# Optimization experiments

Measured on AMD Instinct MI355X. Metric: run time of the kernel, lower is better.

The kernel has to match this reference:

```python
import jax, jax.numpy as jnp
import numpy as np

N, E, D, H = 50000, 800000, 128, 8
C = D // H  # head dim = 16

def _layer_norm(x, g, b, eps=1e-5):
    mu = jnp.mean(x, axis=-1, keepdims=True)
    var = jnp.var(x, axis=-1, keepdims=True)
    return (x - mu) * jax.lax.rsqrt(var + eps) * g + b

def setup_inputs() -> dict:
    key = jax.random.key(0)
    ks = jax.random.split(key, 24)
    def lin(i, fan_in=D):
        s = 1.0 / np.sqrt(fan_in)
        return (jax.random.uniform(ks[i], (D, D), minval=-s, maxval=s),
                jax.random.uniform(ks[i + 1], (D,), minval=-s, maxval=s))
    Wq, bq = lin(0); Wk, bk = lin(2); Wv, bv = lin(4)
    We, be = lin(6); Ws, bs = lin(8)
    W1, b1 = lin(10); W2, b2 = lin(12)
    return {
        'edge_index': jax.random.randint(ks[14], (2, E), 0, N),
        'node_attr': jax.random.normal(ks[15], (N, D), dtype=jnp.float32),
        'edge_attr': jax.random.normal(ks[16], (E, D), dtype=jnp.float32),
        'Wq': Wq, 'bq': bq, 'Wk': Wk, 'bk': bk, 'Wv': Wv, 'bv': bv,
        'We': We, 'be': be, 'Ws': Ws, 'bs': bs,
        'W1': W1, 'b1': b1, 'W2': W2, 'b2': b2,
        'ln1_g': jnp.ones((D,)), 'ln1_b': jnp.zeros((D,)),
        'ln2_g': jnp.ones((D,)), 'ln2_b': jnp.zeros((D,)),
    }

def _transformer_conv(node_attr, edge_attr, src, dst, Wq, bq, Wk, bk, Wv, bv, We, be, Ws, bs):
    # PyG TransformerConv, concat=True, root_weight=True, beta=False, eval (no dropout)
    q = (node_attr @ Wq.T + bq).reshape(N, H, C)[dst]          # [E,H,C]
    e = (edge_attr @ We.T + be).reshape(E, H, C)               # [E,H,C]
    k = (node_attr @ Wk.T + bk).reshape(N, H, C)[src] + e      # [E,H,C]
    v = (node_attr @ Wv.T + bv).reshape(N, H, C)[src] + e      # [E,H,C]
    alpha = jnp.sum(q * k, axis=-1) / jnp.sqrt(jnp.float32(C)) # [E,H]
    # segment softmax over destination node
    m = jax.ops.segment_max(alpha, dst, num_segments=N)        # [N,H]
    ex = jnp.exp(alpha - m[dst])
    denom = jax.ops.segment_sum(ex, dst, num_segments=N)       # [N,H]
    a = ex / (denom[dst] + 1e-16)                              # [E,H]
    out = jax.ops.segment_sum(v * a[..., None], dst, num_segments=N)  # [N,H,C]
    out = out.reshape(N, D)
    return out + node_attr @ Ws.T + bs  # root/skip connection

def reference(edge_index, node_attr, edge_attr, Wq, bq, Wk, bk, Wv, bv, We, be,
              Ws, bs, W1, b1, W2, b2, ln1_g, ln1_b, ln2_g, ln2_b):
    src, dst = edge_index[0], edge_index[1]
    x = _transformer_conv(node_attr, edge_attr, src, dst,
                          Wq, bq, Wk, bk, Wv, bv, We, be, Ws, bs)
    node_attr = node_attr + _layer_norm(x, ln1_g, ln1_b)
    h = jax.nn.silu(node_attr @ W1.T + b1) @ W2.T + b2
    node_attr = node_attr + _layer_norm(h, ln2_g, ln2_b)
    return node_attr
```

## Files before the change

### kernel.cpp

```cpp
#include <hip/hip_runtime.h>
#include <hip/hip_fp16.h>

#define N_NODES 50000
#define N_EDGES 800000
#define DIM 128
#define NODE_TILES 782
#define EDGE_TILES 12500
#define SCAN_NB 50

typedef _Float16 f16;
typedef _Float16 f16x2 __attribute__((ext_vector_type(2)));
typedef _Float16 f16x4 __attribute__((ext_vector_type(4)));
typedef _Float16 f16x8 __attribute__((ext_vector_type(8)));
typedef float    f32x16 __attribute__((ext_vector_type(16)));

__device__ __forceinline__ void sfence() { __builtin_amdgcn_sched_barrier(0); }

__device__ __forceinline__ void load_wfrag(const f16* __restrict__ Wh, int ch, int l31, int g,
                                           f16x8 bf[2][8]) {
#pragma unroll
  for (int c = 0; c < 2; ++c)
#pragma unroll
    for (int ks = 0; ks < 8; ++ks)
      bf[c][ks] = *(const f16x8*)(Wh + ((ch * 64 + c * 32 + l31) << 7) + 16 * ks + 8 * g);
}

__device__ __forceinline__ void stage_issue(const float* __restrict__ X, long M, long base,
                                            int tid, float4 sv[8]) {
#pragma unroll
  for (int kk = 0; kk < 8; ++kk) {
    int i = tid + kk * 256;
    long row = base + (i >> 5);
    long gr = row < M ? row : (M - 1);
    sv[kk] = *(const float4*)(X + gr * DIM + (i & 31) * 4);
  }
}

__device__ __forceinline__ void stage_write(const float4 sv[8], int tid, f16* __restrict__ lds) {
#pragma unroll
  for (int kk = 0; kk < 8; ++kk) {
    int i = tid + kk * 256;
    int r = i >> 5, s8 = i & 31;
    f16x4 h;
    h[0] = (f16)sv[kk].x; h[1] = (f16)sv[kk].y; h[2] = (f16)sv[kk].z; h[3] = (f16)sv[kk].w;
    *(f16x4*)(lds + r * 128 + (((s8 >> 1) ^ (r & 15)) << 3) + ((s8 & 1) << 2)) = h;
  }
}

__device__ __forceinline__ void mfma_lds_g(const f16* __restrict__ A, int lr, int g,
                                           const f16x8 bf[2][8], f32x16 acc[2]) {
#pragma unroll
  for (int c = 0; c < 2; ++c)
#pragma unroll
    for (int k = 0; k < 16; ++k) acc[c][k] = 0.0f;
#pragma unroll
  for (int ks = 0; ks < 8; ++ks) {
    f16x8 a = *(const f16x8*)(A + lr * 128 + (((2 * ks + g) ^ (lr & 15)) << 3));
    acc[0] = __builtin_amdgcn_mfma_f32_32x32x16_f16(a, bf[0][ks], acc[0], 0, 0, 0);
    acc[1] = __builtin_amdgcn_mfma_f32_32x32x16_f16(a, bf[1][ks], acc[1], 0, 0, 0);
  }
}

__device__ __forceinline__ void load_wfrag1(const f16* __restrict__ Wh, int cc, int l31, int g,
                                            f16x8 bf[8]) {
#pragma unroll
  for (int ks = 0; ks < 8; ++ks)
    bf[ks] = *(const f16x8*)(Wh + ((cc * 32 + l31) << 7) + 16 * ks + 8 * g);
}

__device__ __forceinline__ void stage_issue512(const float* __restrict__ X, long M, long base,
                                               int tid, float4 sv[4]) {
#pragma unroll
  for (int kk = 0; kk < 4; ++kk) {
    int i = tid + kk * 512;
    long row = base + (i >> 5);
    long gr = row < M ? row : (M - 1);
    sv[kk] = *(const float4*)(X + gr * DIM + (i & 31) * 4);
  }
}

__device__ __forceinline__ void stage_issue_g512(const float* __restrict__ X,
                                                 const int* __restrict__ elist, long base,
                                                 int tid, float4 sv[4]) {
#pragma unroll
  for (int kk = 0; kk < 4; ++kk) {
    int i = tid + kk * 512;
    int eid = elist[base + (i >> 5)];
    sv[kk] = *(const float4*)(X + (long)eid * DIM + (i & 31) * 4);
  }
}

__device__ __forceinline__ void stage_write512(const float4 sv[4], int tid,
                                               f16* __restrict__ lds) {
#pragma unroll
  for (int kk = 0; kk < 4; ++kk) {
    int i = tid + kk * 512;
    int r = i >> 5, s8 = i & 31;
    f16x4 h;
    h[0] = (f16)sv[kk].x; h[1] = (f16)sv[kk].y; h[2] = (f16)sv[kk].z; h[3] = (f16)sv[kk].w;
    *(f16x4*)(lds + r * 128 + (((s8 >> 1) ^ (r & 15)) << 3) + ((s8 & 1) << 2)) = h;
  }
}

__device__ __forceinline__ void mfma1(const f16* __restrict__ A, int lr, int g,
                                      const f16x8 bf[8], f32x16& acc) {
#pragma unroll
  for (int k = 0; k < 16; ++k) acc[k] = 0.0f;
#pragma unroll
  for (int ks = 0; ks < 8; ++ks) {
    f16x8 a = *(const f16x8*)(A + lr * 128 + (((2 * ks + g) ^ (lr & 15)) << 3));
    acc = __builtin_amdgcn_mfma_f32_32x32x16_f16(a, bf[ks], acc, 0, 0, 0);
  }
}

template <int HALF_OUT>
__device__ __forceinline__ void gemm_store1(const f32x16& acc, long M,
                                            const float* __restrict__ Bv,
                                            void* __restrict__ OUT,
                                            long tile0, int rc, int cc, int l31, int g) {
  int col = cc * 32 + l31;
  float bv = Bv[col];
#pragma unroll
  for (int r = 0; r < 16; ++r) {
    long gm = tile0 + rc * 32 + ((r & 3) + 8 * (r >> 2) + 4 * g);
    if (gm < M) {
      float v = acc[r] + bv;
      if (HALF_OUT) ((f16*)OUT)[gm * DIM + col] = (f16)v;
      else          ((float*)OUT)[gm * DIM + col] = v;
    }
  }
}

__global__ __launch_bounds__(512, 4) void big_gemms(const float* __restrict__ X,
    const float* __restrict__ EA, const int* __restrict__ elist,
    const f16* __restrict__ WhAll,
    const float* __restrict__ bq, const float* __restrict__ bk,
    const float* __restrict__ bv_, const float* __restrict__ bs, const float* __restrict__ be,
    f16* __restrict__ Q, f16* __restrict__ K, f16* __restrict__ V, float* __restrict__ S,
    f16* __restrict__ emat) {
  __shared__ f16 lbuf[64 * 128];
  int tid = threadIdx.x;
  int lane = tid & 63, w = tid >> 6;
  int rc = w >> 2, cc = w & 3, l31 = lane & 31, g = lane >> 5;
  int lr = rc * 32 + l31;

  if (blockIdx.x < NODE_TILES) {
    long tile0 = (long)blockIdx.x * 64;
    float4 sv[4];
    stage_issue512(X, N_NODES, tile0, tid, sv);
    stage_write512(sv, tid, lbuf);
    __syncthreads();
#pragma unroll 1
    for (int mat = 0; mat < 4; ++mat) {
      f16x8 bf[8];
      load_wfrag1(WhAll + mat * 16384, cc, l31, g, bf);
      f32x16 acc;
      mfma1(lbuf, lr, g, bf, acc);
      if (mat == 0)      gemm_store1<1>(acc, N_NODES, bq, Q, tile0, rc, cc, l31, g);
      else if (mat == 1) gemm_store1<1>(acc, N_NODES, bk, K, tile0, rc, cc, l31, g);
      else if (mat == 2) gemm_store1<1>(acc, N_NODES, bv_, V, tile0, rc, cc, l31, g);
      else               gemm_store1<0>(acc, N_NODES, bs, S, tile0, rc, cc, l31, g);
    }
    return;
  }

  long tile0 = (long)(blockIdx.x - NODE_TILES) * 64;
  float4 sv[4];
  stage_issue_g512(EA, elist, tile0, tid, sv);
  sfence();
  stage_write512(sv, tid, lbuf);
  __syncthreads();
  f16x8 bf[8];
  load_wfrag1(WhAll + 4 * 16384, cc, l31, g, bf);
  f32x16 acc;
  mfma1(lbuf, lr, g, bf, acc);
  gemm_store1<1>(acc, (long)N_EDGES, be, emat, tile0, rc, cc, l31, g);
}

__global__ __launch_bounds__(256) void mlp_ln(const float* __restrict__ X,
    const f16* __restrict__ W1h, const float* __restrict__ b1,
    const f16* __restrict__ W2h, const float* __restrict__ b2,
    const float* __restrict__ gv, const float* __restrict__ bv,
    float* __restrict__ outp) {
  __shared__ float smem[64 * 128];
  f16* xs = (f16*)smem;
  f16* hs = (f16*)smem + 64 * 128;
  float* wbuf = smem;
  int tid = threadIdx.x;
  int lane = tid & 63, w = tid >> 6;
  int rc = w >> 1, ch = w & 1, l31 = lane & 31, g = lane >> 5;
  int t = blockIdx.x;
  if (t >= NODE_TILES) return;
  long tile0 = (long)t * 64;
  int lr = rc * 32 + l31;

  float4 sv[8];
  stage_issue(X, N_NODES, tile0, tid, sv);
  f16x8 bf1[2][8];
  load_wfrag(W1h, ch, l31, g, bf1);
  stage_write(sv, tid, xs);
  __syncthreads();

  f32x16 acc[2];
  mfma_lds_g(xs, lr, g, bf1, acc);
  f16x8 bf2[2][8];
  load_wfrag(W2h, ch, l31, g, bf2);

#pragma unroll
  for (int c = 0; c < 2; ++c) {
    int col = ch * 64 + c * 32 + l31;
    float bb = b1[col];
#pragma unroll
    for (int r = 0; r < 16; ++r) {
      int row = rc * 32 + (r & 3) + 8 * (r >> 2) + 4 * g;
      float v = acc[c][r] + bb;
      v = v / (1.0f + __expf(-v));
      hs[row * 128 + (((col >> 3) ^ (row & 15)) << 3) + (col & 7)] = (f16)v;
    }
  }
  __syncthreads();

  f32x16 a2[2];
  mfma_lds_g(hs, lr, g, bf2, a2);
  __syncthreads();

#pragma unroll
  for (int c = 0; c < 2; ++c) {
    int col = ch * 64 + c * 32 + l31;
    float bb = b2[col];
#pragma unroll
    for (int r = 0; r < 16; ++r) {
      int row = rc * 32 + (r & 3) + 8 * (r >> 2) + 4 * g;
      wbuf[row * 128 + col] = a2[c][r] + bb;
    }
  }
  __syncthreads();

  float2 gg = *(const float2*)(gv + 2 * lane);
  float2 bb2 = *(const float2*)(bv + 2 * lane);
#pragma unroll 1
  for (int rr = 0; rr < 16; ++rr) {
    int row = w * 16 + rr;
    long gm = tile0 + row;
    if (gm >= N_NODES) break;
    float2 x;
    x.x = wbuf[row * 128 + 2 * lane];
    x.y = wbuf[row * 128 + 2 * lane + 1];
    float sm = x.x + x.y;
    for (int m = 1; m < 64; m <<= 1) sm += __shfl_xor(sm, m);
    float mu = sm * (1.f / 128.f);
    float dx = x.x - mu, dy = x.y - mu;
    float ss = dx * dx + dy * dy;
    for (int m = 1; m < 64; m <<= 1) ss += __shfl_xor(ss, m);
    float r = rsqrtf(ss * (1.f / 128.f) + 1e-5f);
    float2 bs = *(const float2*)(X + gm * DIM + 2 * lane);
    float2 o;
    o.x = bs.x + dx * r * gg.x + bb2.x;
    o.y = bs.y + dy * r * gg.y + bb2.y;
    *(float2*)(outp + gm * DIM + 2 * lane) = o;
  }
}

__global__ void hist_conv_k(const int* __restrict__ ei, int* __restrict__ counts,
                            const float* __restrict__ a0, const float* __restrict__ a1,
                            const float* __restrict__ a2, const float* __restrict__ a3,
                            const float* __restrict__ a4, const float* __restrict__ a5,
                            const float* __restrict__ a6, f16* __restrict__ dst) {
  long gid = blockIdx.x * 256L + threadIdx.x;
  if (gid < 7 * 16384) {
    int mat = (int)(gid >> 14), el = (int)(gid & 16383);
    const float* s = (mat == 0) ? a0 : (mat == 1) ? a1 : (mat == 2) ? a2 : (mat == 3) ? a3
                   : (mat == 4) ? a4 : (mat == 5) ? a5 : a6;
    dst[gid] = (f16)s[el];
  }
  for (long e = gid; e < N_EDGES; e += 1024L * 256)
    atomicAdd(&counts[ei[N_EDGES + e]], 1);
}

__global__ __launch_bounds__(1024) void blocksum_k(const int* __restrict__ counts,
                                                   int* __restrict__ bsum) {
  __shared__ int sd[1024];
  int t = threadIdx.x, b = blockIdx.x;
  int v = (t < 1000) ? counts[b * 1000 + t] : 0;
  sd[t] = v; __syncthreads();
  for (int off = 512; off > 0; off >>= 1) {
    if (t < off) sd[t] += sd[t + off];
    __syncthreads();
  }
  if (t == 0) bsum[b] = sd[0];
}

__global__ void scan_small(const int* __restrict__ bsum, int* __restrict__ boff,
                           int* __restrict__ offs) {
  if (threadIdx.x == 0) {
    int run = 0;
    for (int b = 0; b < SCAN_NB; ++b) { boff[b] = run; run += bsum[b]; }
    boff[SCAN_NB] = run;
    offs[N_NODES] = run;
  }
}

__global__ __launch_bounds__(1024) void expand_k(const int* __restrict__ counts,
                                                 const int* __restrict__ boff,
                                                 int* __restrict__ offs, int* __restrict__ cursor) {
  __shared__ int sd[1024];
  int t = threadIdx.x, b = blockIdx.x;
  int v = (t < 1000) ? counts[b * 1000 + t] : 0;
  sd[t] = v; __syncthreads();
  for (int off = 1; off < 1024; off <<= 1) {
    int x = (t >= off) ? sd[t - off] : 0;
    __syncthreads();
    sd[t] += x;
    __syncthreads();
  }
  if (t < 1000) {
    int o = boff[b] + sd[t] - v;
    int idx = b * 1000 + t;
    offs[idx] = o;
    cursor[idx] = o;
  }
}

__global__ void scatter_k(const int* __restrict__ ei, int* __restrict__ cursor,
                          int* __restrict__ elist, int* __restrict__ srcs) {
  for (long e = blockIdx.x * (long)blockDim.x + threadIdx.x; e < N_EDGES;
       e += (long)gridDim.x * blockDim.x) {
    int d = ei[N_EDGES + e];
    int pos = atomicAdd(&cursor[d], 1);
    elist[pos] = (int)e;
    srcs[pos] = ei[e];
  }
}

__global__ __launch_bounds__(256) void attn_ln(const int* __restrict__ offs,
    const int* __restrict__ srcs, const f16* __restrict__ emat, const f16* __restrict__ Qn,
    const f16* __restrict__ Kn, const f16* __restrict__ Vn,
    const float* __restrict__ Skip, const float* __restrict__ base,
    const float* __restrict__ gv, const float* __restrict__ bv,
    float* __restrict__ outp) {
  int n = blockIdx.x * 4 + (threadIdx.x >> 6);
  if (n >= N_NODES) return;
  int lane = threadIdx.x & 63;
  int grp = lane >> 4, li = lane & 15;
  int c8 = 8 * li;

  float q[8];
  {
    f16x8 qv = *(const f16x8*)(Qn + (long)n * DIM + c8);
#pragma unroll
    for (int k = 0; k < 8; ++k) q[k] = (float)qv[k];
  }

  int rs = offs[n], re = offs[n + 1];
  float a[8];
#pragma unroll
  for (int k = 0; k < 8; ++k) a[k] = 0.f;
  float den = 0.f;

  if (rs < re) {
    int e0 = rs + grp;
    int sCur = srcs[(e0 < re) ? e0 : (re - 1)];
    for (int i = rs; i < re; i += 4) {
      int ei_ = i + grp;
      bool valid = ei_ < re;
      int ec = valid ? ei_ : (re - 1);
      int s = sCur;
      int en = ei_ + 4;
      sCur = srcs[(en < re) ? en : (re - 1)];
      f16x8 e8 = *(const f16x8*)(emat + (long)ec * DIM + c8);
      f16x8 k8 = *(const f16x8*)(Kn + (long)s * DIM + c8);
      f16x8 v8 = *(const f16x8*)(Vn + (long)s * DIM + c8);
      float p = 0.f;
#pragma unroll
      for (int k = 0; k < 8; ++k) p += q[k] * ((float)k8[k] + (float)e8[k]);
      p += __shfl_xor(p, 1);
      float ex = valid ? __expf(p * 0.25f) : 0.f;
      den += ex;
#pragma unroll
      for (int k = 0; k < 8; ++k) a[k] += ex * ((float)e8[k] + (float)v8[k]);
    }
  }
#pragma unroll
  for (int k = 0; k < 8; ++k) {
    a[k] += __shfl_xor(a[k], 16);
    a[k] += __shfl_xor(a[k], 32);
  }
  den += __shfl_xor(den, 16);
  den += __shfl_xor(den, 32);

  float inv = 1.f / (den + 1e-16f);
  float x[8];
  {
    float4 sk0 = *(const float4*)(Skip + (long)n * DIM + c8);
    float4 sk1 = *(const float4*)(Skip + (long)n * DIM + c8 + 4);
    x[0] = a[0] * inv + sk0.x; x[1] = a[1] * inv + sk0.y;
    x[2] = a[2] * inv + sk0.z; x[3] = a[3] * inv + sk0.w;
    x[4] = a[4] * inv + sk1.x; x[5] = a[5] * inv + sk1.y;
    x[6] = a[6] * inv + sk1.z; x[7] = a[7] * inv + sk1.w;
  }

  float sm = 0.f;
#pragma unroll
  for (int k = 0; k < 8; ++k) sm += x[k];
  for (int m = 1; m < 16; m <<= 1) sm += __shfl_xor(sm, m);
  float mu = sm * (1.f / 128.f);
  float d[8], ss = 0.f;
#pragma unroll
  for (int k = 0; k < 8; ++k) { d[k] = x[k] - mu; ss += d[k] * d[k]; }
  for (int m = 1; m < 16; m <<= 1) ss += __shfl_xor(ss, m);
  float r = rsqrtf(ss * (1.f / 128.f) + 1e-5f);

  if (grp == 0) {
    float4 g0 = *(const float4*)(gv + c8);
    float4 g1 = *(const float4*)(gv + c8 + 4);
    float4 b0 = *(const float4*)(bv + c8);
    float4 b1 = *(const float4*)(bv + c8 + 4);
    float4 s0 = *(const float4*)(base + (long)n * DIM + c8);
    float4 s1 = *(const float4*)(base + (long)n * DIM + c8 + 4);
    float4 o0, o1;
    o0.x = s0.x + d[0] * r * g0.x + b0.x;
    o0.y = s0.y + d[1] * r * g0.y + b0.y;
    o0.z = s0.z + d[2] * r * g0.z + b0.z;
    o0.w = s0.w + d[3] * r * g0.w + b0.w;
    o1.x = s1.x + d[4] * r * g1.x + b1.x;
    o1.y = s1.y + d[5] * r * g1.y + b1.y;
    o1.z = s1.z + d[6] * r * g1.z + b1.z;
    o1.w = s1.w + d[7] * r * g1.w + b1.w;
    *(float4*)(outp + (long)n * DIM + c8) = o0;
    *(float4*)(outp + (long)n * DIM + c8 + 4) = o1;
  }
}

extern "C" void kernel_launch(void* const* d_in, const int* in_sizes, int n_in,
                              void* d_out, int out_size, void* d_ws, size_t ws_size,
                              hipStream_t stream) {
  (void)in_sizes; (void)n_in; (void)out_size; (void)ws_size;
  const int*   ei  = (const int*)d_in[0];
  const float* x0  = (const float*)d_in[1];
  const float* ea  = (const float*)d_in[2];
  const float* Wq  = (const float*)d_in[3];  const float* bq = (const float*)d_in[4];
  const float* Wk  = (const float*)d_in[5];  const float* bk = (const float*)d_in[6];
  const float* Wv  = (const float*)d_in[7];  const float* bv = (const float*)d_in[8];
  const float* We  = (const float*)d_in[9];  const float* be = (const float*)d_in[10];
  const float* Wsk = (const float*)d_in[11]; const float* bsk = (const float*)d_in[12];
  const float* W1  = (const float*)d_in[13]; const float* b1 = (const float*)d_in[14];
  const float* W2  = (const float*)d_in[15]; const float* b2 = (const float*)d_in[16];
  const float* g1  = (const float*)d_in[17]; const float* lb1 = (const float*)d_in[18];
  const float* g2  = (const float*)d_in[19]; const float* lb2 = (const float*)d_in[20];

  char* ws = (char*)d_ws;
  f16*   Qn     = (f16*)(ws + 0);
  f16*   Kn     = (f16*)(ws + 12800000L);
  f16*   Vn     = (f16*)(ws + 25600000L);
  float* Skip   = (float*)(ws + 38400000L);
  int*   offs   = (int*)(ws + 64000000L);
  int*   cursor = (int*)(ws + 64200192L);
  int*   counts = (int*)(ws + 64429568L);
  int*   bsum   = (int*)(ws + 64629760L);
  int*   boff   = bsum + 64;
  int*   elist  = (int*)(ws + 64630272L);
  int*   srcs   = (int*)(ws + 67830272L);
  f16*   emat   = (f16*)(ws + 71030272L);
  float* node1  = (float*)(ws + 275830272L);
  f16*   WhAll  = (f16*)(ws + 301430272L);

  (void)hipMemsetAsync(counts, 0, N_NODES * sizeof(int), stream);
  hist_conv_k<<<1024, 256, 0, stream>>>(ei, counts, Wq, Wk, Wv, Wsk, We, W1, W2, WhAll);
  blocksum_k<<<SCAN_NB, 1024, 0, stream>>>(counts, bsum);
  scan_small<<<1, 64, 0, stream>>>(bsum, boff, offs);
  expand_k<<<SCAN_NB, 1024, 0, stream>>>(counts, boff, offs, cursor);
  scatter_k<<<1024, 256, 0, stream>>>(ei, cursor, elist, srcs);

  big_gemms<<<NODE_TILES + EDGE_TILES, 512, 0, stream>>>(
      x0, ea, elist, WhAll, bq, bk, bv, bsk, be, Qn, Kn, Vn, Skip, emat);
  attn_ln<<<12500, 256, 0, stream>>>(offs, srcs, emat, Qn, Kn, Vn, Skip, x0, g1, lb1, node1);
  mlp_ln<<<NODE_TILES, 256, 0, stream>>>(node1, WhAll + 5 * 16384, b1,
                                         WhAll + 6 * 16384, b2, g2, lb2, (float*)d_out);
}
```

Baseline: 456.0 us.

## Read edge features coalesced and scatter projected edge rows to CSR positions

Instead of gathering edge_attr rows through a dst-sorted edge list (random fp32 reads), the edge GEMM now reads edge_attr sequentially and writes each projected fp16 row to its CSR slot using a per-edge position array produced by the scatter kernel. The output is staged through LDS so each row is written as 16-byte vectors. This swaps scattered 512-byte fp32 reads for scattered 256-byte fp16 writes, adding two block barriers and an extra LDS round-trip per tile.

```diff
diff --git a/kernel.cpp b/kernel.cpp
--- a/kernel.cpp
+++ b/kernel.cpp
@@ -76,17 +76,6 @@
     long row = base + (i >> 5);
     long gr = row < M ? row : (M - 1);
     sv[kk] = *(const float4*)(X + gr * DIM + (i & 31) * 4);
-  }
-}
-
-__device__ __forceinline__ void stage_issue_g512(const float* __restrict__ X,
-                                                 const int* __restrict__ elist, long base,
-                                                 int tid, float4 sv[4]) {
-#pragma unroll
-  for (int kk = 0; kk < 4; ++kk) {
-    int i = tid + kk * 512;
-    int eid = elist[base + (i >> 5)];
-    sv[kk] = *(const float4*)(X + (long)eid * DIM + (i & 31) * 4);
   }
 }
 
@@ -132,13 +121,14 @@
 }
 
 __global__ __launch_bounds__(512, 4) void big_gemms(const float* __restrict__ X,
-    const float* __restrict__ EA, const int* __restrict__ elist,
+    const float* __restrict__ EA, const int* __restrict__ dstpos,
     const f16* __restrict__ WhAll,
     const float* __restrict__ bq, const float* __restrict__ bk,
     const float* __restrict__ bv_, const float* __restrict__ bs, const float* __restrict__ be,
     f16* __restrict__ Q, f16* __restrict__ K, f16* __restrict__ V, float* __restrict__ S,
     f16* __restrict__ emat) {
   __shared__ f16 lbuf[64 * 128];
+  __shared__ int dlds[64];
   int tid = threadIdx.x;
   int lane = tid & 63, w = tid >> 6;
   int rc = w >> 2, cc = w & 3, l31 = lane & 31, g = lane >> 5;
@@ -166,15 +156,34 @@
 
   long tile0 = (long)(blockIdx.x - NODE_TILES) * 64;
   float4 sv[4];
-  stage_issue_g512(EA, elist, tile0, tid, sv);
-  sfence();
+  stage_issue512(EA, (long)N_EDGES, tile0, tid, sv);
+  if (tid < 64) dlds[tid] = dstpos[tile0 + tid];
   stage_write512(sv, tid, lbuf);
   __syncthreads();
   f16x8 bf[8];
   load_wfrag1(WhAll + 4 * 16384, cc, l31, g, bf);
   f32x16 acc;
   mfma1(lbuf, lr, g, bf, acc);
-  gemm_store1<1>(acc, (long)N_EDGES, be, emat, tile0, rc, cc, l31, g);
+  __syncthreads();
+
+  {
+    int col = cc * 32 + l31;
+    float bv = be[col];
+#pragma unroll
+    for (int r = 0; r < 16; ++r) {
+      int row = rc * 32 + (r & 3) + 8 * (r >> 2) + 4 * g;
+      lbuf[row * 128 + col] = (f16)(acc[r] + bv);
+    }
+  }
+  __syncthreads();
+
+#pragma unroll
+  for (int kk = 0; kk < 2; ++kk) {
+    int i = tid + kk * 512;
+    int row = i >> 4, sl = i & 15;
+    long dpos = dlds[row];
+    *(f16x8*)(emat + dpos * 128 + sl * 8) = *(const f16x8*)(lbuf + row * 128 + sl * 8);
+  }
 }
 
 __global__ __launch_bounds__(256) void mlp_ln(const float* __restrict__ X,
@@ -322,13 +331,13 @@
 }
 
 __global__ void scatter_k(const int* __restrict__ ei, int* __restrict__ cursor,
-                          int* __restrict__ elist, int* __restrict__ srcs) {
+                          int* __restrict__ srcs, int* __restrict__ dstpos) {
   for (long e = blockIdx.x * (long)blockDim.x + threadIdx.x; e < N_EDGES;
        e += (long)gridDim.x * blockDim.x) {
     int d = ei[N_EDGES + e];
     int pos = atomicAdd(&cursor[d], 1);
-    elist[pos] = (int)e;
     srcs[pos] = ei[e];
+    dstpos[e] = pos;
   }
 }
 
@@ -458,8 +467,8 @@
   int*   counts = (int*)(ws + 64429568L);
   int*   bsum   = (int*)(ws + 64629760L);
   int*   boff   = bsum + 64;
-  int*   elist  = (int*)(ws + 64630272L);
-  int*   srcs   = (int*)(ws + 67830272L);
+  int*   srcs   = (int*)(ws + 64630272L);
+  int*   dstpos = (int*)(ws + 67830272L);
   f16*   emat   = (f16*)(ws + 71030272L);
   float* node1  = (float*)(ws + 275830272L);
   f16*   WhAll  = (f16*)(ws + 301430272L);
@@ -469,10 +478,10 @@
   blocksum_k<<<SCAN_NB, 1024, 0, stream>>>(counts, bsum);
   scan_small<<<1, 64, 0, stream>>>(bsum, boff, offs);
   expand_k<<<SCAN_NB, 1024, 0, stream>>>(counts, boff, offs, cursor);
-  scatter_k<<<1024, 256, 0, stream>>>(ei, cursor, elist, srcs);
+  scatter_k<<<1024, 256, 0, stream>>>(ei, cursor, srcs, dstpos);
 
   big_gemms<<<NODE_TILES + EDGE_TILES, 512, 0, stream>>>(
-      x0, ea, elist, WhAll, bq, bk, bv, bsk, be, Qn, Kn, Vn, Skip, emat);
+      x0, ea, dstpos, WhAll, bq, bk, bv, bsk, be, Qn, Kn, Vn, Skip, emat);
   attn_ln<<<12500, 256, 0, stream>>>(offs, srcs, emat, Qn, Kn, Vn, Skip, x0, g1, lb1, node1);
   mlp_ln<<<NODE_TILES, 256, 0, stream>>>(node1, WhAll + 5 * 16384, b1,
                                          WhAll + 6 * 16384, b2, g2, lb2, (float*)d_out);
```

Result: slower. 478.3 us (+4.9%).

## Read edge features contiguously in GEMM and gather emat by edge id in attention

Applied to the files above, without the earlier changes.

The edge projection GEMM now streams edge_attr in original edge order instead of gathering rows through the CSR edge list, and writes emat in original order. The attention kernel then gathers half-precision emat rows through a packed (src, edge id) int2 metadata array built by the scatter kernel. This moves the random gather from fp32 input rows to smaller fp16 rows and removes a dependent index load before the GEMM staging. The cost is random rather than sequential emat reads in attention, plus a wider per-edge metadata load.

```diff
diff --git a/kernel.cpp b/kernel.cpp
--- a/kernel.cpp
+++ b/kernel.cpp
@@ -76,17 +76,6 @@
     long row = base + (i >> 5);
     long gr = row < M ? row : (M - 1);
     sv[kk] = *(const float4*)(X + gr * DIM + (i & 31) * 4);
-  }
-}
-
-__device__ __forceinline__ void stage_issue_g512(const float* __restrict__ X,
-                                                 const int* __restrict__ elist, long base,
-                                                 int tid, float4 sv[4]) {
-#pragma unroll
-  for (int kk = 0; kk < 4; ++kk) {
-    int i = tid + kk * 512;
-    int eid = elist[base + (i >> 5)];
-    sv[kk] = *(const float4*)(X + (long)eid * DIM + (i & 31) * 4);
   }
 }
 
@@ -132,7 +121,7 @@
 }
 
 __global__ __launch_bounds__(512, 4) void big_gemms(const float* __restrict__ X,
-    const float* __restrict__ EA, const int* __restrict__ elist,
+    const float* __restrict__ EA,
     const f16* __restrict__ WhAll,
     const float* __restrict__ bq, const float* __restrict__ bk,
     const float* __restrict__ bv_, const float* __restrict__ bs, const float* __restrict__ be,
@@ -166,8 +155,7 @@
 
   long tile0 = (long)(blockIdx.x - NODE_TILES) * 64;
   float4 sv[4];
-  stage_issue_g512(EA, elist, tile0, tid, sv);
-  sfence();
+  stage_issue512(EA, (long)N_EDGES, tile0, tid, sv);
   stage_write512(sv, tid, lbuf);
   __syncthreads();
   f16x8 bf[8];
@@ -322,18 +310,17 @@
 }
 
 __global__ void scatter_k(const int* __restrict__ ei, int* __restrict__ cursor,
-                          int* __restrict__ elist, int* __restrict__ srcs) {
+                          int2* __restrict__ meta) {
   for (long e = blockIdx.x * (long)blockDim.x + threadIdx.x; e < N_EDGES;
        e += (long)gridDim.x * blockDim.x) {
     int d = ei[N_EDGES + e];
     int pos = atomicAdd(&cursor[d], 1);
-    elist[pos] = (int)e;
-    srcs[pos] = ei[e];
+    meta[pos] = make_int2(ei[e], (int)e);
   }
 }
 
 __global__ __launch_bounds__(256) void attn_ln(const int* __restrict__ offs,
-    const int* __restrict__ srcs, const f16* __restrict__ emat, const f16* __restrict__ Qn,
+    const int2* __restrict__ meta, const f16* __restrict__ emat, const f16* __restrict__ Qn,
     const f16* __restrict__ Kn, const f16* __restrict__ Vn,
     const float* __restrict__ Skip, const float* __restrict__ base,
     const float* __restrict__ gv, const float* __restrict__ bv,
@@ -359,15 +346,15 @@
 
   if (rs < re) {
     int e0 = rs + grp;
-    int sCur = srcs[(e0 < re) ? e0 : (re - 1)];
+    int2 mCur = meta[(e0 < re) ? e0 : (re - 1)];
     for (int i = rs; i < re; i += 4) {
       int ei_ = i + grp;
       bool valid = ei_ < re;
-      int ec = valid ? ei_ : (re - 1);
-      int s = sCur;
+      int s = mCur.x;
+      long eid = mCur.y;
       int en = ei_ + 4;
-      sCur = srcs[(en < re) ? en : (re - 1)];
-      f16x8 e8 = *(const f16x8*)(emat + (long)ec * DIM + c8);
+      mCur = meta[(en < re) ? en : (re - 1)];
+      f16x8 e8 = *(const f16x8*)(emat + eid * DIM + c8);
       f16x8 k8 = *(const f16x8*)(Kn + (long)s * DIM + c8);
       f16x8 v8 = *(const f16x8*)(Vn + (long)s * DIM + c8);
       float p = 0.f;
@@ -458,8 +445,7 @@
   int*   counts = (int*)(ws + 64429568L);
   int*   bsum   = (int*)(ws + 64629760L);
   int*   boff   = bsum + 64;
-  int*   elist  = (int*)(ws + 64630272L);
-  int*   srcs   = (int*)(ws + 67830272L);
+  int2*  meta   = (int2*)(ws + 64630272L);
   f16*   emat   = (f16*)(ws + 71030272L);
   float* node1  = (float*)(ws + 275830272L);
   f16*   WhAll  = (f16*)(ws + 301430272L);
@@ -469,11 +455,11 @@
   blocksum_k<<<SCAN_NB, 1024, 0, stream>>>(counts, bsum);
   scan_small<<<1, 64, 0, stream>>>(bsum, boff, offs);
   expand_k<<<SCAN_NB, 1024, 0, stream>>>(counts, boff, offs, cursor);
-  scatter_k<<<1024, 256, 0, stream>>>(ei, cursor, elist, srcs);
+  scatter_k<<<1024, 256, 0, stream>>>(ei, cursor, meta);
 
   big_gemms<<<NODE_TILES + EDGE_TILES, 512, 0, stream>>>(
-      x0, ea, elist, WhAll, bq, bk, bv, bsk, be, Qn, Kn, Vn, Skip, emat);
-  attn_ln<<<12500, 256, 0, stream>>>(offs, srcs, emat, Qn, Kn, Vn, Skip, x0, g1, lb1, node1);
+      x0, ea, WhAll, bq, bk, bv, bsk, be, Qn, Kn, Vn, Skip, emat);
+  attn_ln<<<12500, 256, 0, stream>>>(offs, meta, emat, Qn, Kn, Vn, Skip, x0, g1, lb1, node1);
   mlp_ln<<<NODE_TILES, 256, 0, stream>>>(node1, WhAll + 5 * 16384, b1,
                                          WhAll + 6 * 16384, b2, g2, lb2, (float*)d_out);
 }
```

Result: no change. 447.7 us, median of 2 (-1.8%).
